# Kernel tuning notes

Measured on AMD Instinct MI355X. Metric: run time of the kernel, lower is better.

## Reference

```python
import jax, jax.numpy as jnp
import numpy as np
from jax import lax

N = 8192      # nodes == batch (forward cats node and batch embeddings)
E = 262144    # edges, avg degree 32
T = 32        # seq_len
DD = 16       # dynamic_feature_dim
DS = 128      # static_feature_dim
GH = 64       # gnn_hidden_dim
RH = 128      # rnn_hidden_dim
L = 10        # output_lead_times
EPS = 1e-5


def setup_inputs() -> dict:
    key = jax.random.key(0)
    ks = jax.random.split(key, 32)
    def rn(i, shape, s=0.05):
        return jax.random.normal(ks[i], shape, jnp.float32) * s
    return {
        "dynamic_features": rn(0, (N, T, DD), 1.0),
        "x_static": rn(1, (N, DS), 1.0),
        "edge_index": jax.random.randint(ks[2], (2, E), 0, N, jnp.int32),
        "gcn1_w": rn(3, (DS, GH)), "gcn1_b": rn(4, (GH,)),
        "gcn2_w": rn(5, (GH, GH)), "gcn2_b": rn(6, (GH,)),
        "bn1_g": 1.0 + rn(7, (GH,)), "bn1_b": rn(8, (GH,)),
        "bn2_g": 1.0 + rn(9, (GH,)), "bn2_b": rn(10, (GH,)),
        "w_ih0": rn(11, (4 * RH, DD)), "w_hh0": rn(12, (4 * RH, RH)),
        "b_ih0": rn(13, (4 * RH,)), "b_hh0": rn(14, (4 * RH,)),
        "w_ih1": rn(15, (4 * RH, RH)), "w_hh1": rn(16, (4 * RH, RH)),
        "b_ih1": rn(17, (4 * RH,)), "b_hh1": rn(18, (4 * RH,)),
        "fc1_w": rn(19, (GH + RH, 128)), "fc1_b": rn(20, (128,)),
        "fbn_g": 1.0 + rn(21, (128,)), "fbn_b": rn(22, (128,)),
        "fc2_w": rn(23, (128, 64)), "fc2_b": rn(24, (64,)),
        "out_w": rn(25, (64, L)), "out_b": rn(26, (L,)),
    }


def _gcn(x, w, b, src, dst, n):
    h = x @ w
    loops = jnp.arange(n, dtype=src.dtype)
    s = jnp.concatenate([src, loops])
    d = jnp.concatenate([dst, loops])
    deg = jax.ops.segment_sum(jnp.ones(s.shape[0], x.dtype), d, num_segments=n)
    dis = lax.rsqrt(jnp.maximum(deg, 1.0))
    msg = h[s] * (dis[s] * dis[d])[:, None]
    return jax.ops.segment_sum(msg, d, num_segments=n) + b


def _bn(x, g, b):
    # eval-mode BatchNorm1d: running_mean=0, running_var=1
    return x * (g * lax.rsqrt(jnp.asarray(1.0 + EPS, x.dtype))) + b


def _lstm_layer(xp, w_hh):
    # xp: [B, T, 4H] input projection with both biases already added
    B = xp.shape[0]
    H = w_hh.shape[1]
    h0 = jnp.zeros((B, H), xp.dtype)
    c0 = jnp.zeros((B, H), xp.dtype)
    def step(carry, xt):
        h, c = carry
        gates = xt + h @ w_hh.T  # torch gate order: i, f, g, o
        i, f, g, o = jnp.split(gates, 4, axis=-1)
        c = jax.nn.sigmoid(f) * c + jax.nn.sigmoid(i) * jnp.tanh(g)
        h = jax.nn.sigmoid(o) * jnp.tanh(c)
        return (h, c), h
    _, hs = lax.scan(step, (h0, c0), jnp.swapaxes(xp, 0, 1))
    return jnp.swapaxes(hs, 0, 1)  # [B, T, H]


def _forward(dynamic_features, x_static, edge_index,
             gcn1_w, gcn1_b, gcn2_w, gcn2_b, bn1_g, bn1_b, bn2_g, bn2_b,
             w_ih0, w_hh0, b_ih0, b_hh0, w_ih1, w_hh1, b_ih1, b_hh1,
             fc1_w, fc1_b, fbn_g, fbn_b, fc2_w, fc2_b, out_w, out_b):
    src, dst = edge_index[0], edge_index[1]
    n = x_static.shape[0]
    # GNN branch (dropout = eval-mode identity)
    h = _gcn(x_static, gcn1_w, gcn1_b, src, dst, n)
    h = jax.nn.relu(_bn(h, bn1_g, bn1_b))
    h = _gcn(h, gcn2_w, gcn2_b, src, dst, n)
    gnn_emb = jax.nn.relu(_bn(h, bn2_g, bn2_b))
    # 2-layer LSTM branch
    xp0 = jnp.einsum('btd,gd->btg', dynamic_features, w_ih0) + b_ih0 + b_hh0
    h1 = _lstm_layer(xp0, w_hh0)
    xp1 = jnp.einsum('bth,gh->btg', h1, w_ih1) + b_ih1 + b_hh1
    h2 = _lstm_layer(xp1, w_hh1)
    rnn_emb = h2[:, -1, :]
    # fusion MLP
    fused = jnp.concatenate([gnn_emb, rnn_emb], axis=1)
    x = jax.nn.relu(_bn(fused @ fc1_w + fc1_b, fbn_g, fbn_b))
    x = jax.nn.relu(x @ fc2_w + fc2_b)
    return x @ out_w + out_b


def reference(dynamic_features, x_static, edge_index,
              gcn1_w, gcn1_b, gcn2_w, gcn2_b, bn1_g, bn1_b, bn2_g, bn2_b,
              w_ih0, w_hh0, b_ih0, b_hh0, w_ih1, w_hh1, b_ih1, b_hh1,
              fc1_w, fc1_b, fbn_g, fbn_b, fc2_w, fc2_b, out_w, out_b):
    return _forward(dynamic_features, x_static, edge_index,
                    gcn1_w, gcn1_b, gcn2_w, gcn2_b, bn1_g, bn1_b, bn2_g, bn2_b,
                    w_ih0, w_hh0, b_ih0, b_hh0, w_ih1, w_hh1, b_ih1, b_hh1,
                    fc1_w, fc1_b, fbn_g, fbn_b, fc2_w, fc2_b, out_w, out_b)
```

## Files before the change

kernel.cpp:

```cpp
#include <hip/hip_runtime.h>
#include <hip/hip_bf16.h>

#define NN 8192
#define NE 262144

typedef float v2 __attribute__((ext_vector_type(2)));
typedef float v4 __attribute__((ext_vector_type(4)));
typedef float f4 __attribute__((ext_vector_type(4)));
typedef _Float16 h8 __attribute__((ext_vector_type(8)));
typedef _Float16 h4 __attribute__((ext_vector_type(4)));

__device__ __forceinline__ float rcp_(float x) { return __builtin_amdgcn_rcpf(x); }
__device__ __forceinline__ float sigm(float x) { return rcp_(1.0f + __expf(-x)); }
__device__ __forceinline__ float tanh_(float x) { return 1.0f - 2.0f * rcp_(__expf(2.0f * x) + 1.0f); }

__global__ void k_prep_all(const float* __restrict__ dyn,
                           const float* __restrict__ wih0, const float* __restrict__ whh0,
                           const float* __restrict__ bih0, const float* __restrict__ bhh0,
                           const float* __restrict__ wih1, const float* __restrict__ whh1,
                           const float* __restrict__ bih1, const float* __restrict__ bhh1,
                           const int* __restrict__ dst,
                           const float* __restrict__ xs_, const float* __restrict__ g1w,
                           _Float16* __restrict__ dyn16, _Float16* __restrict__ WB0h,
                           _Float16* __restrict__ TLg, _Float16* __restrict__ WB1,
                           float* __restrict__ bias, int* __restrict__ cnt,
                           float* __restrict__ hs_raw) {
    int b = blockIdx.x, tid = threadIdx.x;
    if (b < 4096) {
        int i = b * 256 + tid;
        f4 v = *(const f4*)(dyn + (size_t)i * 4);
        h4 o = {(_Float16)v[0], (_Float16)v[1], (_Float16)v[2], (_Float16)v[3]};
        *(h4*)(dyn16 + (size_t)i * 4) = o;
    } else if (b < 4900) {
        int i = (b - 4096) * 256 + tid;
        if (i < 65536) {
            int idx = i & 7, col = (i >> 3) & 511, kgq = (i >> 12) & 3, kt = i >> 14;
            int kh = kt * 32 + kgq * 8 + idx;
            WB0h[i] = (_Float16)whh0[col * 128 + kh];
        } else if (i < 73728) {
            int m = i - 65536;
            int kd = m & 15, g = m >> 4;
            TLg[m] = (_Float16)wih0[g * 16 + kd];
        } else if (i < 204800) {
            int m = i - 73728;
            int kt = m >> 14, rem = m & 16383, g = rem >> 5, kk = rem & 31, k = kt * 32 + kk;
            WB1[m] = (_Float16)((k < 128) ? wih1[g * 128 + k] : whh1[g * 128 + (k - 128)]);
        } else {
            int g = i - 204800;
            bias[g] = (g < 512) ? (bih0[g] + bhh0[g]) : (bih1[g - 512] + bhh1[g - 512]);
        }
    } else if (b < 5924) {
        int e = (b - 4900) * 256 + tid;
        if (e < NE) atomicAdd(&cnt[dst[e]], 1);
    } else {
        int wv = tid >> 6, ln = tid & 63;
        int row = (b - 5924) * 4 + wv;
        const float* xp = xs_ + (size_t)row * 128;
        float a = 0.f;
#pragma unroll 4
        for (int k = 0; k < 128; ++k) a += xp[k] * g1w[k * 64 + ln];
        hs_raw[(size_t)row * 64 + ln] = a;
    }
}

__global__ __launch_bounds__(1024) void k_scan(const int* __restrict__ cnt, int* __restrict__ rowstart,
                                               float* __restrict__ dis) {
    __shared__ int part[1024];
    int t = threadIdx.x;
    int base = t * 8, s = 0, loc[8];
#pragma unroll
    for (int i = 0; i < 8; ++i) { loc[i] = s; s += cnt[base + i]; }
    part[t] = s;
    __syncthreads();
    for (int off = 1; off < 1024; off <<= 1) {
        int v = part[t];
        int add = (t >= off) ? part[t - off] : 0;
        __syncthreads();
        part[t] = v + add;
        __syncthreads();
    }
    int pre = (t == 0) ? 0 : part[t - 1];
#pragma unroll
    for (int i = 0; i < 8; ++i) {
        rowstart[base + i] = pre + loc[i];
        dis[base + i] = rsqrtf((float)(cnt[base + i] + 1));
    }
    if (t == 1023) rowstart[8192] = NE;
}
__global__ void k_fill(const int* __restrict__ src, const int* __restrict__ dst,
                       const int* __restrict__ rowstart, int* __restrict__ cursor,
                       int* __restrict__ srcidx) {
    int e = blockIdx.x * 256 + threadIdx.x;
    if (e < NE) {
        int d = dst[e];
        int pos = rowstart[d] + atomicAdd(&cursor[d], 1);
        srcidx[pos] = src[e];
    }
}
__global__ __launch_bounds__(256) void k_gather_gemm(const float* __restrict__ hs, const int* __restrict__ srcidx,
                                                     const int* __restrict__ rowstart, const float* __restrict__ dis,
                                                     const float* __restrict__ gb, const float* __restrict__ bng,
                                                     const float* __restrict__ bnb, const float* __restrict__ g2w,
                                                     float* __restrict__ hs2) {
    int ln = threadIdx.x & 63;
    int d = (blockIdx.x * 256 + threadIdx.x) >> 6;
    float dd = dis[d];
    float acc = hs[(size_t)d * 64 + ln] * dd;
    int b = rowstart[d], e = rowstart[d + 1];
    int i = b;
    for (; i + 4 <= e; i += 4) {
        int s0 = srcidx[i], s1 = srcidx[i + 1], s2 = srcidx[i + 2], s3 = srcidx[i + 3];
        acc += hs[(size_t)s0 * 64 + ln] * dis[s0];
        acc += hs[(size_t)s1 * 64 + ln] * dis[s1];
        acc += hs[(size_t)s2 * 64 + ln] * dis[s2];
        acc += hs[(size_t)s3 * 64 + ln] * dis[s3];
    }
    for (; i < e; ++i) { int s = srcidx[i]; acc += hs[(size_t)s * 64 + ln] * dis[s]; }
    float rs = rsqrtf(1.0f + 1e-5f);
    float y = acc * dd + gb[ln];
    y = fmaxf(y * (bng[ln] * rs) + bnb[ln], 0.f);
    float a2 = 0.f;
#pragma unroll 8
    for (int k = 0; k < 64; ++k) a2 += __shfl(y, k, 64) * g2w[k * 64 + ln];
    hs2[(size_t)d * 64 + ln] = a2;
}
__global__ __launch_bounds__(256) void k_gather(const float* __restrict__ hs, const int* __restrict__ srcidx,
                                                const int* __restrict__ rowstart, const float* __restrict__ dis,
                                                const float* __restrict__ gb, const float* __restrict__ bng,
                                                const float* __restrict__ bnb, float* __restrict__ out) {
    int ln = threadIdx.x & 63;
    int d = (blockIdx.x * 256 + threadIdx.x) >> 6;
    float dd = dis[d];
    float acc = hs[(size_t)d * 64 + ln] * dd;
    int b = rowstart[d], e = rowstart[d + 1];
    int i = b;
    for (; i + 4 <= e; i += 4) {
        int s0 = srcidx[i], s1 = srcidx[i + 1], s2 = srcidx[i + 2], s3 = srcidx[i + 3];
        acc += hs[(size_t)s0 * 64 + ln] * dis[s0];
        acc += hs[(size_t)s1 * 64 + ln] * dis[s1];
        acc += hs[(size_t)s2 * 64 + ln] * dis[s2];
        acc += hs[(size_t)s3 * 64 + ln] * dis[s3];
    }
    for (; i < e; ++i) { int s = srcidx[i]; acc += hs[(size_t)s * 64 + ln] * dis[s]; }
    float rs = rsqrtf(1.0f + 1e-5f);
    float v = acc * dd + gb[ln];
    v = v * (bng[ln] * rs) + bnb[ln];
    out[(size_t)d * 64 + ln] = fmaxf(v, 0.f);
}

__device__ __forceinline__ h8 ldx(const _Float16* xs, int buf, int row, int chunk) {
    return *(const h8*)((const char*)xs + buf * 16384 + row * 512 + ((chunk ^ (row & 7)) << 4));
}
__device__ __forceinline__ void wrx(_Float16* xs, int buf, int row, int col, _Float16 v) {
    *(_Float16*)((char*)xs + buf * 16384 + row * 512 + ((((col >> 3) ^ (row & 7))) << 4) + (col & 7) * 2) = v;
}

__global__ __launch_bounds__(512, 2) void k_lstm(const _Float16* __restrict__ dyn16,
                                                 const _Float16* __restrict__ WB0h,
                                                 const _Float16* __restrict__ TLg,
                                                 const _Float16* __restrict__ WB1,
                                                 const float* __restrict__ bias,
                                                 float* __restrict__ rnn) {
    __shared__ __align__(16) _Float16 wb0[65536];
    __shared__ __align__(16) _Float16 xs[16384];

    const int tid = threadIdx.x;
    const int wv = tid >> 6, ln = tid & 63;
    const int lr = ln & 15, kg = ln >> 4;
    const int j = wv * 16 + lr;
    const int row0 = blockIdx.x * 32;

    for (int i = tid; i < 8192; i += 512) ((v4*)wb0)[i] = ((const v4*)WB0h)[i];
    for (int i = tid; i < 16384; i += 512) xs[i] = (_Float16)0.f;

    h8 b1r[8][4];
#pragma unroll
    for (int kt = 0; kt < 8; ++kt)
#pragma unroll
        for (int q = 0; q < 4; ++q)
            b1r[kt][q] = *(const h8*)(WB1 + (size_t)kt * 16384 + (q * 128 + j) * 32 + kg * 8);
    h8 bt[4];
#pragma unroll
    for (int q = 0; q < 4; ++q)
        bt[q] = *(const h8*)(TLg + (q * 128 + j) * 16 + (kg & 1) * 8);

    float b0q[4], b1q[4];
#pragma unroll
    for (int q = 0; q < 4; ++q) { b0q[q] = bias[q * 128 + j]; b1q[q] = bias[512 + q * 128 + j]; }
    float c0[2][4], c1[2][4];
#pragma unroll
    for (int mt = 0; mt < 2; ++mt)
#pragma unroll
        for (int r = 0; r < 4; ++r) { c0[mt][r] = 0.f; c1[mt][r] = 0.f; }

    h8 dreg[2], pre[2];
#pragma unroll
    for (int mt = 0; mt < 2; ++mt)
#pragma unroll
        for (int e = 0; e < 8; ++e) { dreg[mt][e] = (_Float16)0.f; pre[mt][e] = (_Float16)0.f; }
    if (kg < 2) {
#pragma unroll
        for (int mt = 0; mt < 2; ++mt)
            dreg[mt] = *(const h8*)(dyn16 + (size_t)(row0 + mt * 16 + lr) * 512 + (kg & 1) * 8);
    }
    __syncthreads();

    {
        f4 acc[2][4];
#pragma unroll
        for (int q = 0; q < 4; ++q) { f4 z = {b0q[q], b0q[q], b0q[q], b0q[q]}; acc[0][q] = z; acc[1][q] = z; }
#pragma unroll
        for (int q = 0; q < 4; ++q) {
            acc[0][q] = __builtin_amdgcn_mfma_f32_16x16x32_f16(dreg[0], bt[q], acc[0][q], 0, 0, 0);
            acc[1][q] = __builtin_amdgcn_mfma_f32_16x16x32_f16(dreg[1], bt[q], acc[1][q], 0, 0, 0);
        }
#pragma unroll
        for (int mt = 0; mt < 2; ++mt)
#pragma unroll
            for (int r = 0; r < 4; ++r) {
                float iv = acc[mt][0][r], fv = acc[mt][1][r], gv = acc[mt][2][r], ov = acc[mt][3][r];
                float c = sigm(fv) * c0[mt][r] + sigm(iv) * tanh_(gv);
                c0[mt][r] = c;
                wrx(xs, 0, mt * 16 + kg * 4 + r, j, (_Float16)(sigm(ov) * tanh_(c)));
            }
        if (kg < 2) {
#pragma unroll
            for (int mt = 0; mt < 2; ++mt)
                dreg[mt] = *(const h8*)(dyn16 + (size_t)(row0 + mt * 16 + lr) * 512 + 16 + (kg & 1) * 8);
        }
    }

#pragma unroll 1
    for (int i = 0; i < 31; ++i) {
        const int cur = i & 1, old = cur ^ 1;
        __syncthreads();
        if (i < 30 && kg < 2) {
#pragma unroll
            for (int mt = 0; mt < 2; ++mt)
                pre[mt] = *(const h8*)(dyn16 + (size_t)(row0 + mt * 16 + lr) * 512 + (i + 2) * 16 + (kg & 1) * 8);
        }
        f4 acc[2][4];
#pragma unroll
        for (int q = 0; q < 4; ++q) { f4 z = {b1q[q], b1q[q], b1q[q], b1q[q]}; acc[0][q] = z; acc[1][q] = z; }
#pragma unroll
        for (int kt = 0; kt < 8; ++kt) {
            const int bufA = (kt < 4) ? cur : old;
            const int ch = (kt < 4) ? (kt * 4 + kg) : (16 + (kt - 4) * 4 + kg);
            h8 a0 = ldx(xs, bufA, lr, ch);
            h8 a1 = ldx(xs, bufA, 16 + lr, ch);
#pragma unroll
            for (int q = 0; q < 4; ++q) {
                acc[0][q] = __builtin_amdgcn_mfma_f32_16x16x32_f16(a0, b1r[kt][q], acc[0][q], 0, 0, 0);
                acc[1][q] = __builtin_amdgcn_mfma_f32_16x16x32_f16(a1, b1r[kt][q], acc[1][q], 0, 0, 0);
            }
        }
#pragma unroll
        for (int mt = 0; mt < 2; ++mt)
#pragma unroll
            for (int r = 0; r < 4; ++r) {
                float iv = acc[mt][0][r], fv = acc[mt][1][r], gv = acc[mt][2][r], ov = acc[mt][3][r];
                float c = sigm(fv) * c1[mt][r] + sigm(iv) * tanh_(gv);
                c1[mt][r] = c;
                wrx(xs, cur, mt * 16 + kg * 4 + r, 128 + j, (_Float16)(sigm(ov) * tanh_(c)));
            }
#pragma unroll
        for (int q = 0; q < 4; ++q) { f4 z = {b0q[q], b0q[q], b0q[q], b0q[q]}; acc[0][q] = z; acc[1][q] = z; }
#pragma unroll
        for (int kt = 0; kt < 4; ++kt) {
            h8 a0 = ldx(xs, cur, lr, kt * 4 + kg);
            h8 a1 = ldx(xs, cur, 16 + lr, kt * 4 + kg);
            h8 bq[4];
#pragma unroll
            for (int q = 0; q < 4; ++q)
                bq[q] = *(const h8*)(wb0 + (size_t)(((kt * 4 + kg) * 512 + q * 128 + j) * 8));
#pragma unroll
            for (int q = 0; q < 4; ++q) {
                acc[0][q] = __builtin_amdgcn_mfma_f32_16x16x32_f16(a0, bq[q], acc[0][q], 0, 0, 0);
                acc[1][q] = __builtin_amdgcn_mfma_f32_16x16x32_f16(a1, bq[q], acc[1][q], 0, 0, 0);
            }
        }
#pragma unroll
        for (int q = 0; q < 4; ++q) {
            acc[0][q] = __builtin_amdgcn_mfma_f32_16x16x32_f16(dreg[0], bt[q], acc[0][q], 0, 0, 0);
            acc[1][q] = __builtin_amdgcn_mfma_f32_16x16x32_f16(dreg[1], bt[q], acc[1][q], 0, 0, 0);
        }
#pragma unroll
        for (int mt = 0; mt < 2; ++mt)
#pragma unroll
            for (int r = 0; r < 4; ++r) {
                float iv = acc[mt][0][r], fv = acc[mt][1][r], gv = acc[mt][2][r], ov = acc[mt][3][r];
                float c = sigm(fv) * c0[mt][r] + sigm(iv) * tanh_(gv);
                c0[mt][r] = c;
                wrx(xs, old, mt * 16 + kg * 4 + r, j, (_Float16)(sigm(ov) * tanh_(c)));
            }
        if (i < 30) { dreg[0] = pre[0]; dreg[1] = pre[1]; }
    }
    __syncthreads();
    {
        const int cur = 1, old = 0;
        f4 acc[2][4];
#pragma unroll
        for (int q = 0; q < 4; ++q) { f4 z = {b1q[q], b1q[q], b1q[q], b1q[q]}; acc[0][q] = z; acc[1][q] = z; }
#pragma unroll
        for (int kt = 0; kt < 8; ++kt) {
            const int bufA = (kt < 4) ? cur : old;
            const int ch = (kt < 4) ? (kt * 4 + kg) : (16 + (kt - 4) * 4 + kg);
            h8 a0 = ldx(xs, bufA, lr, ch);
            h8 a1 = ldx(xs, bufA, 16 + lr, ch);
#pragma unroll
            for (int q = 0; q < 4; ++q) {
                acc[0][q] = __builtin_amdgcn_mfma_f32_16x16x32_f16(a0, b1r[kt][q], acc[0][q], 0, 0, 0);
                acc[1][q] = __builtin_amdgcn_mfma_f32_16x16x32_f16(a1, b1r[kt][q], acc[1][q], 0, 0, 0);
            }
        }
#pragma unroll
        for (int mt = 0; mt < 2; ++mt)
#pragma unroll
            for (int r = 0; r < 4; ++r) {
                float iv = acc[mt][0][r], fv = acc[mt][1][r], gv = acc[mt][2][r], ov = acc[mt][3][r];
                float c = sigm(fv) * c1[mt][r] + sigm(iv) * tanh_(gv);
                float h = sigm(ov) * tanh_(c);
                rnn[(size_t)(row0 + mt * 16 + kg * 4 + r) * 128 + j] = h;
            }
    }
}

__global__ __launch_bounds__(256) void k_head(const float* __restrict__ gnn, const float* __restrict__ rnn,
                                              const float* __restrict__ fc1w, const float* __restrict__ fc1b,
                                              const float* __restrict__ fbng, const float* __restrict__ fbnb,
                                              const float* __restrict__ fc2w, const float* __restrict__ fc2b,
                                              const float* __restrict__ outw, const float* __restrict__ outb,
                                              float* __restrict__ out) {
    __shared__ __align__(16) float xin[32][196];
    __shared__ __align__(16) float xh2[32][132];
    __shared__ __align__(16) float xh3[32][68];
    const int tid = threadIdx.x;
    const int r0 = blockIdx.x * 32;
    for (int i = tid; i < 32 * 64; i += 256) { int r = i >> 6, c = i & 63; xin[r][c] = gnn[(size_t)(r0 + r) * 64 + c]; }
    for (int i = tid; i < 32 * 128; i += 256) { int r = i >> 7, c = i & 127; xin[r][64 + c] = rnn[(size_t)(r0 + r) * 128 + c]; }
    __syncthreads();
    const int wv = tid >> 6, ln = tid & 63, wr = wv * 8;
    const float rs = rsqrtf(1.0f + 1e-5f);
    float a[8][2];
    float b0 = fc1b[2 * ln], b1 = fc1b[2 * ln + 1];
#pragma unroll
    for (int r = 0; r < 8; ++r) { a[r][0] = b0; a[r][1] = b1; }
    for (int k = 0; k < 192; ++k) {
        v2 w = *(const v2*)&fc1w[k * 128 + 2 * ln];
#pragma unroll
        for (int r = 0; r < 8; ++r) { float x = xin[wr + r][k]; a[r][0] += x * w[0]; a[r][1] += x * w[1]; }
    }
    float s0 = fbng[2 * ln] * rs, s1 = fbng[2 * ln + 1] * rs;
    float bb0 = fbnb[2 * ln], bb1 = fbnb[2 * ln + 1];
#pragma unroll
    for (int r = 0; r < 8; ++r) {
        v2 h;
        h[0] = fmaxf(a[r][0] * s0 + bb0, 0.f);
        h[1] = fmaxf(a[r][1] * s1 + bb1, 0.f);
        *(v2*)&xh2[wr + r][2 * ln] = h;
    }
    __syncthreads();
    float a2[8];
    float b2 = fc2b[ln];
#pragma unroll
    for (int r = 0; r < 8; ++r) a2[r] = b2;
    for (int k = 0; k < 128; ++k) {
        float w = fc2w[k * 64 + ln];
#pragma unroll
        for (int r = 0; r < 8; ++r) a2[r] += xh2[wr + r][k] * w;
    }
#pragma unroll
    for (int r = 0; r < 8; ++r) xh3[wr + r][ln] = fmaxf(a2[r], 0.f);
    __syncthreads();
    if (ln < 10) {
#pragma unroll
        for (int r = 0; r < 8; ++r) {
            float a3 = outb[ln];
            for (int k = 0; k < 64; ++k) a3 += xh3[wr + r][k] * outw[k * 10 + ln];
            out[(size_t)(r0 + wr + r) * 10 + ln] = a3;
        }
    }
}

extern "C" void kernel_launch(void* const* d_in, const int* in_sizes, int n_in,
                              void* d_out, int out_size, void* d_ws, size_t ws_size,
                              hipStream_t stream) {
    const float* dyn  = (const float*)d_in[0];
    const float* xs_  = (const float*)d_in[1];
    const int*   ei   = (const int*)d_in[2];
    const float* g1w  = (const float*)d_in[3];
    const float* g1b  = (const float*)d_in[4];
    const float* g2w  = (const float*)d_in[5];
    const float* g2b  = (const float*)d_in[6];
    const float* bn1g = (const float*)d_in[7];
    const float* bn1b = (const float*)d_in[8];
    const float* bn2g = (const float*)d_in[9];
    const float* bn2b = (const float*)d_in[10];
    const float* wih0 = (const float*)d_in[11];
    const float* whh0 = (const float*)d_in[12];
    const float* bih0 = (const float*)d_in[13];
    const float* bhh0 = (const float*)d_in[14];
    const float* wih1 = (const float*)d_in[15];
    const float* whh1 = (const float*)d_in[16];
    const float* bih1 = (const float*)d_in[17];
    const float* bhh1 = (const float*)d_in[18];
    const float* fc1w = (const float*)d_in[19];
    const float* fc1b = (const float*)d_in[20];
    const float* fbng = (const float*)d_in[21];
    const float* fbnb = (const float*)d_in[22];
    const float* fc2w = (const float*)d_in[23];
    const float* fc2b = (const float*)d_in[24];
    const float* outw = (const float*)d_in[25];
    const float* outb = (const float*)d_in[26];
    float* out = (float*)d_out;

    char* ws = (char*)d_ws;
    _Float16* WB0h  = (_Float16*)(ws + 0);
    _Float16* TLg   = (_Float16*)(ws + 131072);
    _Float16* WB1   = (_Float16*)(ws + 147456);
    _Float16* dyn16 = (_Float16*)(ws + 409600);
    float* fbase = (float*)(ws + 8798208);
    float* bias = fbase;
    float* dis  = fbase + 1024;
    float* hs   = fbase + 9216;
    float* hs2  = fbase + 533504;
    float* gnn  = fbase + 1057792;
    float* rnn  = fbase + 1582080;
    int* ibase   = (int*)(ws + 19320832);
    int* cnt     = ibase;
    int* cursor  = ibase + 8192;
    int* rowstart= ibase + 16384;
    int* srcidx  = ibase + 24592;

    const int* srcp = ei;
    const int* dstp = ei + NE;

    hipMemsetAsync(cnt, 0, 2 * 8192 * sizeof(int), stream);
    k_prep_all<<<7972, 256, 0, stream>>>(dyn, wih0, whh0, bih0, bhh0, wih1, whh1, bih1, bhh1,
                                         dstp, xs_, g1w, dyn16, WB0h, TLg, WB1, bias, cnt, hs);
    k_scan<<<1, 1024, 0, stream>>>(cnt, rowstart, dis);
    k_fill<<<1024, 256, 0, stream>>>(srcp, dstp, rowstart, cursor, srcidx);
    k_gather_gemm<<<2048, 256, 0, stream>>>(hs, srcidx, rowstart, dis, g1b, bn1g, bn1b, g2w, hs2);
    k_gather<<<2048, 256, 0, stream>>>(hs2, srcidx, rowstart, dis, g2b, bn2g, bn2b, gnn);
    k_lstm<<<256, 512, 0, stream>>>(dyn16, WB0h, TLg, WB1, bias, rnn);
    k_head<<<256, 256, 0, stream>>>(gnn, rnn, fc1w, fc1b, fbng, fbnb, fc2w, fc2b, outw, outb, out);
}
```

Measured before the change: 311.2 us.

## Fuse the fusion-MLP head into the LSTM kernel epilogue

Removes the separate head kernel and runs the fc1/BN/fc2/output MLP at the end of the LSTM kernel. The final hidden state goes into LDS reused from the weight buffer instead of a global rnn array, and the gnn embedding is staged alongside it. This saves one launch plus a global write and read of the RNN embedding. The head now runs on 512 threads per block with different per-thread work, adding serial work after the recurrence, which only has 256 blocks. It also replaces the one-step-ahead register prefetch of the dynamic input with a load issued at the end of each step, which can expose more load latency inside the recurrence.

```diff
diff --git a/kernel.cpp b/kernel.cpp
--- a/kernel.cpp
+++ b/kernel.cpp
@@ -160,7 +160,12 @@
                                                  const _Float16* __restrict__ TLg,
                                                  const _Float16* __restrict__ WB1,
                                                  const float* __restrict__ bias,
-                                                 float* __restrict__ rnn) {
+                                                 const float* __restrict__ gnn,
+                                                 const float* __restrict__ fc1w, const float* __restrict__ fc1b,
+                                                 const float* __restrict__ fbng, const float* __restrict__ fbnb,
+                                                 const float* __restrict__ fc2w, const float* __restrict__ fc2b,
+                                                 const float* __restrict__ outw, const float* __restrict__ outb,
+                                                 float* __restrict__ out) {
     __shared__ __align__(16) _Float16 wb0[65536];
     __shared__ __align__(16) _Float16 xs[16384];
 
@@ -193,11 +198,11 @@
 #pragma unroll
         for (int r = 0; r < 4; ++r) { c0[mt][r] = 0.f; c1[mt][r] = 0.f; }
 
-    h8 dreg[2], pre[2];
+    h8 dreg[2];
 #pragma unroll
     for (int mt = 0; mt < 2; ++mt)
 #pragma unroll
-        for (int e = 0; e < 8; ++e) { dreg[mt][e] = (_Float16)0.f; pre[mt][e] = (_Float16)0.f; }
+        for (int e = 0; e < 8; ++e) dreg[mt][e] = (_Float16)0.f;
     if (kg < 2) {
 #pragma unroll
         for (int mt = 0; mt < 2; ++mt)
@@ -234,11 +239,6 @@
     for (int i = 0; i < 31; ++i) {
         const int cur = i & 1, old = cur ^ 1;
         __syncthreads();
-        if (i < 30 && kg < 2) {
-#pragma unroll
-            for (int mt = 0; mt < 2; ++mt)
-                pre[mt] = *(const h8*)(dyn16 + (size_t)(row0 + mt * 16 + lr) * 512 + (i + 2) * 16 + (kg & 1) * 8);
-        }
         f4 acc[2][4];
 #pragma unroll
         for (int q = 0; q < 4; ++q) { f4 z = {b1q[q], b1q[q], b1q[q], b1q[q]}; acc[0][q] = z; acc[1][q] = z; }
@@ -293,9 +293,17 @@
                 c0[mt][r] = c;
                 wrx(xs, old, mt * 16 + kg * 4 + r, j, (_Float16)(sigm(ov) * tanh_(c)));
             }
-        if (i < 30) { dreg[0] = pre[0]; dreg[1] = pre[1]; }
-    }
-    __syncthreads();
+        if (i < 30 && kg < 2) {
+#pragma unroll
+            for (int mt = 0; mt < 2; ++mt)
+                dreg[mt] = *(const h8*)(dyn16 + (size_t)(row0 + mt * 16 + lr) * 512 + (i + 2) * 16 + (kg & 1) * 8);
+        }
+    }
+    __syncthreads();
+    float* hd = (float*)wb0;
+    float* h2 = hd + 6144;
+    float* h3 = h2 + 4096;
+    f4 gstage = *(const f4*)&gnn[(size_t)(row0 + (tid >> 4)) * 64 + (tid & 15) * 4];
     {
         const int cur = 1, old = 0;
         f4 acc[2][4];
@@ -313,6 +321,7 @@
                 acc[1][q] = __builtin_amdgcn_mfma_f32_16x16x32_f16(a1, b1r[kt][q], acc[1][q], 0, 0, 0);
             }
         }
+        *(f4*)&hd[(tid >> 4) * 192 + (tid & 15) * 4] = gstage;
 #pragma unroll
         for (int mt = 0; mt < 2; ++mt)
 #pragma unroll
@@ -320,65 +329,53 @@
                 float iv = acc[mt][0][r], fv = acc[mt][1][r], gv = acc[mt][2][r], ov = acc[mt][3][r];
                 float c = sigm(fv) * c1[mt][r] + sigm(iv) * tanh_(gv);
                 float h = sigm(ov) * tanh_(c);
-                rnn[(size_t)(row0 + mt * 16 + kg * 4 + r) * 128 + j] = h;
-            }
-    }
-}
-
-__global__ __launch_bounds__(256) void k_head(const float* __restrict__ gnn, const float* __restrict__ rnn,
-                                              const float* __restrict__ fc1w, const float* __restrict__ fc1b,
-                                              const float* __restrict__ fbng, const float* __restrict__ fbnb,
-                                              const float* __restrict__ fc2w, const float* __restrict__ fc2b,
-                                              const float* __restrict__ outw, const float* __restrict__ outb,
-                                              float* __restrict__ out) {
-    __shared__ __align__(16) float xin[32][196];
-    __shared__ __align__(16) float xh2[32][132];
-    __shared__ __align__(16) float xh3[32][68];
-    const int tid = threadIdx.x;
-    const int r0 = blockIdx.x * 32;
-    for (int i = tid; i < 32 * 64; i += 256) { int r = i >> 6, c = i & 63; xin[r][c] = gnn[(size_t)(r0 + r) * 64 + c]; }
-    for (int i = tid; i < 32 * 128; i += 256) { int r = i >> 7, c = i & 127; xin[r][64 + c] = rnn[(size_t)(r0 + r) * 128 + c]; }
-    __syncthreads();
-    const int wv = tid >> 6, ln = tid & 63, wr = wv * 8;
-    const float rs = rsqrtf(1.0f + 1e-5f);
-    float a[8][2];
-    float b0 = fc1b[2 * ln], b1 = fc1b[2 * ln + 1];
-#pragma unroll
-    for (int r = 0; r < 8; ++r) { a[r][0] = b0; a[r][1] = b1; }
-    for (int k = 0; k < 192; ++k) {
-        v2 w = *(const v2*)&fc1w[k * 128 + 2 * ln];
-#pragma unroll
-        for (int r = 0; r < 8; ++r) { float x = xin[wr + r][k]; a[r][0] += x * w[0]; a[r][1] += x * w[1]; }
-    }
-    float s0 = fbng[2 * ln] * rs, s1 = fbng[2 * ln + 1] * rs;
-    float bb0 = fbnb[2 * ln], bb1 = fbnb[2 * ln + 1];
-#pragma unroll
-    for (int r = 0; r < 8; ++r) {
-        v2 h;
-        h[0] = fmaxf(a[r][0] * s0 + bb0, 0.f);
-        h[1] = fmaxf(a[r][1] * s1 + bb1, 0.f);
-        *(v2*)&xh2[wr + r][2 * ln] = h;
-    }
-    __syncthreads();
-    float a2[8];
-    float b2 = fc2b[ln];
-#pragma unroll
-    for (int r = 0; r < 8; ++r) a2[r] = b2;
-    for (int k = 0; k < 128; ++k) {
-        float w = fc2w[k * 64 + ln];
-#pragma unroll
-        for (int r = 0; r < 8; ++r) a2[r] += xh2[wr + r][k] * w;
-    }
-#pragma unroll
-    for (int r = 0; r < 8; ++r) xh3[wr + r][ln] = fmaxf(a2[r], 0.f);
-    __syncthreads();
-    if (ln < 10) {
-#pragma unroll
-        for (int r = 0; r < 8; ++r) {
-            float a3 = outb[ln];
-            for (int k = 0; k < 64; ++k) a3 += xh3[wr + r][k] * outw[k * 10 + ln];
-            out[(size_t)(r0 + wr + r) * 10 + ln] = a3;
-        }
+                hd[(mt * 16 + kg * 4 + r) * 192 + 64 + j] = h;
+            }
+    }
+    __syncthreads();
+    const int hr = tid >> 4;
+    const int cg = tid & 15;
+    {
+        float a1[8];
+        const float rs2 = rsqrtf(1.0f + 1e-5f);
+#pragma unroll
+        for (int u = 0; u < 8; ++u) a1[u] = fc1b[cg * 8 + u];
+#pragma unroll 4
+        for (int k = 0; k < 192; ++k) {
+            float x = hd[hr * 192 + k];
+            const float* wr_ = fc1w + k * 128 + cg * 8;
+            f4 w0 = *(const f4*)wr_;
+            f4 w1 = *(const f4*)(wr_ + 4);
+            a1[0] += x * w0[0]; a1[1] += x * w0[1]; a1[2] += x * w0[2]; a1[3] += x * w0[3];
+            a1[4] += x * w1[0]; a1[5] += x * w1[1]; a1[6] += x * w1[2]; a1[7] += x * w1[3];
+        }
+#pragma unroll
+        for (int u = 0; u < 8; ++u) {
+            float v = a1[u] * (fbng[cg * 8 + u] * rs2) + fbnb[cg * 8 + u];
+            h2[hr * 128 + cg * 8 + u] = fmaxf(v, 0.f);
+        }
+    }
+    __syncthreads();
+    {
+        float a2v[4];
+#pragma unroll
+        for (int u = 0; u < 4; ++u) a2v[u] = fc2b[cg * 4 + u];
+#pragma unroll 4
+        for (int k = 0; k < 128; ++k) {
+            float x = h2[hr * 128 + k];
+            f4 w = *(const f4*)&fc2w[k * 64 + cg * 4];
+            a2v[0] += x * w[0]; a2v[1] += x * w[1]; a2v[2] += x * w[2]; a2v[3] += x * w[3];
+        }
+#pragma unroll
+        for (int u = 0; u < 4; ++u) h3[hr * 64 + cg * 4 + u] = fmaxf(a2v[u], 0.f);
+    }
+    __syncthreads();
+    if (tid < 320) {
+        int r = tid / 10, c = tid % 10;
+        float a3 = outb[c];
+#pragma unroll 8
+        for (int k = 0; k < 64; ++k) a3 += h3[r * 64 + k] * outw[k * 10 + c];
+        out[(size_t)(row0 + r) * 10 + c] = a3;
     }
 }
 
@@ -425,7 +422,6 @@
     float* hs   = fbase + 9216;
     float* hs2  = fbase + 533504;
     float* gnn  = fbase + 1057792;
-    float* rnn  = fbase + 1582080;
     int* ibase   = (int*)(ws + 19320832);
     int* cnt     = ibase;
     int* cursor  = ibase + 8192;
@@ -442,6 +438,6 @@
     k_fill<<<1024, 256, 0, stream>>>(srcp, dstp, rowstart, cursor, srcidx);
     k_gather_gemm<<<2048, 256, 0, stream>>>(hs, srcidx, rowstart, dis, g1b, bn1g, bn1b, g2w, hs2);
     k_gather<<<2048, 256, 0, stream>>>(hs2, srcidx, rowstart, dis, g2b, bn2g, bn2b, gnn);
-    k_lstm<<<256, 512, 0, stream>>>(dyn16, WB0h, TLg, WB1, bias, rnn);
-    k_head<<<256, 256, 0, stream>>>(gnn, rnn, fc1w, fc1b, fbng, fbnb, fc2w, fc2b, outw, outb, out);
-}
+    k_lstm<<<256, 512, 0, stream>>>(dyn16, WB0h, TLg, WB1, bias, gnn,
+                                    fc1w, fc1b, fbng, fbnb, fc2w, fc2b, outw, outb, out);
+}
```

Result: faster. 298.6 us (-4.0%).
